# Optimization experiments

Measured on AMD Instinct MI355X. Metric: run time of the kernel, lower is better.

Reference implementation:

```python
import jax, jax.numpy as jnp
import numpy as np

RANK = 32
W0 = 30.0


def lip_linear(x, w, c, b=None):
    # LipschitzLinear: scale rows of w so row-wise L1 norm <= softplus(c)
    scale = jnp.minimum(jax.nn.softplus(c) / jnp.sum(jnp.abs(w), axis=-1), 1.0)
    y = x @ (w * scale[:, None]).T
    return y + b if b is not None else y


def setup_inputs() -> dict:
    key = jax.random.key(0)
    ks = jax.random.split(key, 20)
    d = {}
    d['coords'] = jax.random.normal(ks[0], (8, 32768, 3), dtype=jnp.float32)
    d['latents'] = jax.random.normal(ks[1], (8, 128), dtype=jnp.float32)
    d['nf_w_first'] = jax.random.normal(ks[2], (256, 3), dtype=jnp.float32)
    d['nf_b_first'] = jax.random.normal(ks[3], (256,), dtype=jnp.float32)
    d['nf_c_first'] = jax.random.uniform(ks[4], (1,), dtype=jnp.float32)
    d['nf_w_hid'] = jax.random.normal(ks[5], (3, 256, 256), dtype=jnp.float32)
    d['nf_b_hid'] = jax.random.normal(ks[6], (3, 256), dtype=jnp.float32)
    d['nf_c_hid'] = jax.random.uniform(ks[7], (3,), dtype=jnp.float32)
    d['nf_w_last'] = jax.random.normal(ks[8], (1, 256), dtype=jnp.float32)
    d['nf_b_last'] = jax.random.normal(ks[9], (1,), dtype=jnp.float32)
    d['nf_c_last'] = jax.random.uniform(ks[10], (1,), dtype=jnp.float32)
    d['Aw_first'] = jax.random.normal(ks[11], (96, 128), dtype=jnp.float32)
    d['Ac_first'] = jax.random.uniform(ks[12], (1,), dtype=jnp.float32)
    d['Aw_hid'] = jax.random.normal(ks[13], (3, 8192, 128), dtype=jnp.float32)
    d['Ac_hid'] = jax.random.uniform(ks[14], (3,), dtype=jnp.float32)
    d['Bw'] = jax.random.normal(ks[15], (4, 8192, 128), dtype=jnp.float32)
    d['Bc'] = jax.random.uniform(ks[16], (4,), dtype=jnp.float32)
    d['hbw'] = jax.random.normal(ks[17], (4, 256, 128), dtype=jnp.float32)
    d['hbc'] = jax.random.uniform(ks[18], (4,), dtype=jnp.float32)
    return d


def reference(coords, latents, nf_w_first, nf_b_first, nf_c_first, nf_w_hid, nf_b_hid, nf_c_hid,
              nf_w_last, nf_b_last, nf_c_last, Aw_first, Ac_first, Aw_hid, Ac_hid, Bw, Bc, hbw, hbc):
    T = latents.shape[0]
    # assemble per-layer params: (nf_w, nf_b, nf_c, A_w, A_c, B_w, B_c, hb_w, hb_c)
    layers = [(nf_w_first, nf_b_first, nf_c_first, Aw_first, Ac_first, Bw[0], Bc[0], hbw[0], hbc[0])]
    for j in range(nf_w_hid.shape[0]):
        layers.append((nf_w_hid[j], nf_b_hid[j], nf_c_hid[j], Aw_hid[j], Ac_hid[j],
                       Bw[j + 1], Bc[j + 1], hbw[j + 1], hbc[j + 1]))

    x = coords  # [T, N, d_in]
    for (w, b, c, aw, ac, bw, bc, hw, hc) in layers:
        d_out, d_in = w.shape
        A = lip_linear(latents, aw, ac).reshape(T, d_in, RANK)   # [T, d_in, r]
        B = lip_linear(latents, bw, bc).reshape(T, RANK, d_out)  # [T, r, d_out]
        bias = lip_linear(latents, hw, hc)                       # [T, d_out]
        base = lip_linear(x, w, c, b)                            # [T, N, d_out]
        mod = jnp.einsum('tnr,tro->tno', jnp.einsum('tni,tir->tnr', x, A), B)
        x = jnp.sin(W0 * (base + mod + bias[:, None, :]))
    return lip_linear(x, nf_w_last, nf_c_last, nf_b_last)  # [T, N, 1]
```

## Files before the change

### kernel.cpp

```cpp
#include <hip/hip_runtime.h>
#include <math.h>

#define W0F 30.0f
#define NPTS 32768

#define C_30_OVER_2PI 4.774648292756860070
#define C_2PI         6.283185307179586477

typedef double v4d __attribute__((ext_vector_type(4)));

#define OFF_M     0ull
#define SZ_M      2097152ull
#define OFF_CB    (OFF_M + SZ_M)
#define SZ_CB     8192ull
#define OFF_AF    (OFF_CB + SZ_CB)
#define SZ_AF     262144ull
#define OFF_BF    (OFF_AF + SZ_AF)
#define SZ_BF     262144ull
#define OFF_HB    (OFF_BF + SZ_BF)
#define SZ_HB     8192ull
#define OFF_NSC   (OFF_HB + SZ_HB)
#define SZ_NSC    2048ull
#define OFF_BSWZ  (OFF_NSC + SZ_NSC)
#define SZ_BSWZ   2097152ull
#define OFF_X0    (OFF_BSWZ + SZ_BSWZ)

__global__ __launch_bounds__(256) void setup1(
    const float* __restrict__ latents,
    const float* __restrict__ AwF, const float* __restrict__ AcF,
    const float* __restrict__ AwH, const float* __restrict__ AcH,
    const float* __restrict__ Bw,  const float* __restrict__ Bc,
    const float* __restrict__ hbw, const float* __restrict__ hbc,
    const float* __restrict__ wF,  const float* __restrict__ cF,
    const float* __restrict__ wH,  const float* __restrict__ cH,
    const float* __restrict__ wL,  const float* __restrict__ cL,
    float* __restrict__ AF, float* __restrict__ BFo,
    float* __restrict__ HBo, float* __restrict__ NSC)
{
    __shared__ float lat[1024];
    int tid = threadIdx.x;
    for (int j = tid; j < 1024; j += 256) lat[j] = latents[j];
    __syncthreads();
    int g = blockIdx.x * 256 + tid;
    if (g < 58464) {
        const float* src; float c; float* dst; int stride;
        if (g < 96) {
            src = AwF + g * 128; c = AcF[0]; dst = AF + g; stride = 8192;
        } else if (g < 24672) {
            int q = g - 96; int l = 1 + q / 8192;
            src = AwH + (size_t)q * 128; c = AcH[l - 1];
            dst = AF + (size_t)l * 8 * 8192 + (q % 8192); stride = 8192;
        } else if (g < 57440) {
            int q = g - 24672; int l = q / 8192;
            src = Bw + (size_t)q * 128; c = Bc[l];
            dst = BFo + (size_t)l * 8 * 8192 + (q % 8192); stride = 8192;
        } else {
            int q = g - 57440; int l = q / 256;
            src = hbw + (size_t)q * 128; c = hbc[l];
            dst = HBo + l * 8 * 256 + (q % 256); stride = 256;
        }
        double l1 = 0.0;
        double acc[8] = {0,0,0,0,0,0,0,0};
        for (int kk = 0; kk < 32; ++kk) {
            float4 w4 = ((const float4*)src)[kk];
            l1 += fabs((double)w4.x) + fabs((double)w4.y)
                + fabs((double)w4.z) + fabs((double)w4.w);
            int k = kk * 4;
            #pragma unroll
            for (int t = 0; t < 8; ++t) {
                const float* lp = &lat[t * 128 + k];
                acc[t] = fma((double)w4.x, (double)lp[0], acc[t]);
                acc[t] = fma((double)w4.y, (double)lp[1], acc[t]);
                acc[t] = fma((double)w4.z, (double)lp[2], acc[t]);
                acc[t] = fma((double)w4.w, (double)lp[3], acc[t]);
            }
        }
        double s = fmin(log1p(exp((double)c)) / l1, 1.0);
        #pragma unroll
        for (int t = 0; t < 8; ++t) dst[(size_t)t * stride] = (float)(acc[t] * s);
    } else if (g < 59489) {
        int h = g - 58464;
        if (h < 256) {
            const float* src = wF + h * 3;
            double l1 = fabs((double)src[0]) + fabs((double)src[1]) + fabs((double)src[2]);
            NSC[h] = (float)fmin(log1p(exp((double)cF[0])) / l1, 1.0);
        } else if (h < 1024) {
            int q = h - 256; int l = 1 + q / 256;
            const float* src = wH + (size_t)q * 256;
            double l1 = 0.0;
            for (int kk = 0; kk < 64; ++kk) {
                float4 w4 = ((const float4*)src)[kk];
                l1 += fabs((double)w4.x) + fabs((double)w4.y)
                    + fabs((double)w4.z) + fabs((double)w4.w);
            }
            NSC[256 + q] = (float)fmin(log1p(exp((double)cH[l - 1])) / l1, 1.0);
        } else {
            double l1 = 0.0;
            for (int kk = 0; kk < 64; ++kk) {
                float4 w4 = ((const float4*)wL)[kk];
                l1 += fabs((double)w4.x) + fabs((double)w4.y)
                    + fabs((double)w4.z) + fabs((double)w4.w);
            }
            NSC[1024] = (float)fmin(log1p(exp((double)cL[0])) / l1, 1.0);
        }
    }
}

__global__ __launch_bounds__(256) void setup2(
    const float* __restrict__ wF, const float* __restrict__ bF,
    const float* __restrict__ wH, const float* __restrict__ bH,
    const float* __restrict__ AF, const float* __restrict__ BFi,
    const float* __restrict__ HBi, const float* __restrict__ NSC,
    float* __restrict__ Mb, float* __restrict__ CBb)
{
    int b = blockIdx.x; int t = b / 49; int rem = b % 49;
    int o = threadIdx.x;
    int l, i0, ni;
    if (rem == 0) { l = 0; i0 = 0; ni = 3; }
    else { l = 1 + (rem - 1) / 16; i0 = ((rem - 1) % 16) * 16; ni = 16; }
    size_t ltb = (size_t)(l * 8 + t);
    const float* af = AF + ltb * 8192;
    const float* bf = BFi + ltb * 8192;
    double sc = (double)NSC[l * 256 + o];
    float bcol[32];
    #pragma unroll
    for (int r = 0; r < 32; ++r) bcol[r] = bf[r * 256 + o];
    for (int ii = 0; ii < ni; ++ii) {
        int i = i0 + ii;
        float wv = (l == 0) ? wF[o * 3 + i] : wH[(size_t)((l - 1) * 256 + o) * 256 + i];
        double m = (double)wv * sc;
        #pragma unroll
        for (int r = 0; r < 32; ++r)
            m = fma((double)af[i * 32 + r], (double)bcol[r], m);
        Mb[ltb * 65536 + (size_t)i * 256 + o] = (float)m;
    }
    if (rem == 0 || ((rem - 1) % 16) == 0) {
        double bb = (l == 0) ? (double)bF[o] : (double)bH[(l - 1) * 256 + o];
        CBb[ltb * 256 + o] = (float)(bb + (double)HBi[ltb * 256 + o]);
    }
}

__global__ __launch_bounds__(256) void setup3(
    const float* __restrict__ Mb, float* __restrict__ Bswz)
{
    int gid = blockIdx.x * 256 + threadIdx.x;
    int e    = gid & 3;
    int lane = (gid >> 2) & 63;
    int h    = (gid >> 8) & 1;
    int s    = (gid >> 9) & 63;
    int ltc  = gid >> 15;
    int q = lane >> 4, c16 = lane & 15;
    int ltb = ltc >> 1, ch = ltc & 1;
    int n = h * 4 + e;
    Bswz[gid] = Mb[(size_t)ltb * 65536 + (size_t)(4 * s + q) * 256
                   + ch * 128 + n * 16 + c16];
}

__device__ __forceinline__ float sin30(double z) {
    double u = z * C_30_OVER_2PI;
    double r = u - rint(u);
    return sinf((float)(r * C_2PI));
}

__global__ __launch_bounds__(256) void layer0_k(
    const float* __restrict__ coords, const float* __restrict__ Mb,
    const float* __restrict__ CBb, float* __restrict__ X, int tbase)
{
    __shared__ float Ms[3][256];
    __shared__ float cbs[256];
    int tid = threadIdx.x;
    int tl = blockIdx.x >> 10; int rb = blockIdx.x & 1023;
    int t = tbase + tl;
    const float* Mt = Mb + (size_t)t * 65536;
    Ms[0][tid] = Mt[tid]; Ms[1][tid] = Mt[256 + tid]; Ms[2][tid] = Mt[512 + tid];
    cbs[tid] = CBb[t * 256 + tid];
    __syncthreads();
    int r = rb * 32 + (tid >> 3); int lane8 = tid & 7;
    const float* cp = coords + ((size_t)t * NPTS + r) * 3;
    double c0 = (double)cp[0], c1 = (double)cp[1], c2 = (double)cp[2];
    float* xo = X + ((size_t)tl * NPTS + r) * 256;
#define L0E(col) sin30(fma(c2, (double)Ms[2][col], fma(c1, (double)Ms[1][col], \
                  fma(c0, (double)Ms[0][col], (double)cbs[col]))))
    #pragma unroll
    for (int j = 0; j < 8; ++j) {
        int col = 4 * lane8 + 32 * j;
        float4 v;
        v.x = L0E(col + 0);
        v.y = L0E(col + 1);
        v.z = L0E(col + 2);
        v.w = L0E(col + 3);
        *(float4*)(xo + col) = v;
    }
#undef L0E
}

__global__ __launch_bounds__(256, 4) void gemm_sin(
    const float* __restrict__ Xsrc, float* __restrict__ Xdst,
    const float* __restrict__ Bswz, const float* __restrict__ CBb,
    int l, int tbase)
{
    int tid = threadIdx.x;
    int b = blockIdx.x;
    int tl = b >> 10;
    int rb = (b >> 1) & 511;
    int ch = b & 1;
    size_t ltb = (size_t)(l * 8 + tbase + tl);
    const float* cbp = CBb + ltb * 256 + ch * 128;
    const float* Xs = Xsrc + ((size_t)tl * NPTS + rb * 64) * 256;
    float*       Xd = Xdst + ((size_t)tl * NPTS + rb * 64) * 256 + ch * 128;
    int wave = tid >> 6, lane = tid & 63;
    int q = lane >> 4, c16 = lane & 15;
    v4d zz = {0., 0., 0., 0.};
    v4d p1 = __builtin_amdgcn_mfma_f64_16x16x4f64((double)(1 << c16), 1.0, zz, 0, 0, 0);
    v4d p2 = __builtin_amdgcn_mfma_f64_16x16x4f64(1.0, (double)(1 << c16), zz, 0, 0, 0);
    int r0 = 61 - __builtin_clzll((unsigned long long)p1[0]);
    int r1 = 61 - __builtin_clzll((unsigned long long)p1[1]);
    int r2 = 61 - __builtin_clzll((unsigned long long)p1[2]);
    int r3 = 61 - __builtin_clzll((unsigned long long)p1[3]);
    int c0 = 61 - __builtin_clzll((unsigned long long)p2[0]);
    int c1 = 61 - __builtin_clzll((unsigned long long)p2[1]);
    int c2 = 61 - __builtin_clzll((unsigned long long)p2[2]);
    int c3 = 61 - __builtin_clzll((unsigned long long)p2[3]);
    const float* ap  = Xs + (size_t)(wave * 16 + c16) * 256 + q;
    const float* bzl = Bswz + ((size_t)ltb * 2 + ch) * 32768 + lane * 4;
    v4d acc0 = {0.,0.,0.,0.}, acc1 = {0.,0.,0.,0.}, acc2 = {0.,0.,0.,0.},
        acc3 = {0.,0.,0.,0.}, acc4 = {0.,0.,0.,0.}, acc5 = {0.,0.,0.,0.},
        acc6 = {0.,0.,0.,0.}, acc7 = {0.,0.,0.,0.};
    float  aC  = ap[0];
    float4 bC0 = *(const float4*)(bzl + 0 * 256);
    float4 bC1 = *(const float4*)(bzl + 1 * 256);
    float  aN  = ap[4];
    float4 bN0 = *(const float4*)(bzl + 2 * 256);
    float4 bN1 = *(const float4*)(bzl + 3 * 256);
    #pragma unroll 2
    for (int s = 0; s < 64; ++s) {
        int s2 = (s < 62) ? s + 2 : 63;
        float  aNN  = ap[4 * s2];
        float4 bNN0 = *(const float4*)(bzl + (s2 * 2 + 0) * 256);
        float4 bNN1 = *(const float4*)(bzl + (s2 * 2 + 1) * 256);
        double av = (double)aC;
#define TILE(n, bf) { acc##n = __builtin_amdgcn_mfma_f64_16x16x4f64(          \
                               av, (double)(bf), acc##n, 0, 0, 0); }
        TILE(0, bC0.x) TILE(1, bC0.y) TILE(2, bC0.z) TILE(3, bC0.w)
        TILE(4, bC1.x) TILE(5, bC1.y) TILE(6, bC1.z) TILE(7, bC1.w)
#undef TILE
        aC = aN;  aN = aNN;
        bC0 = bN0; bC1 = bN1; bN0 = bNN0; bN1 = bNN1;
    }
    float* Xw = Xd + (size_t)(wave * 16) * 256;
#define EPT(n) {                                                               \
        int cb0 = (n) * 16;                                                    \
        Xw[r0 * 256 + cb0 + c0] = sin30(acc##n[0] + (double)cbp[cb0 + c0]);    \
        Xw[r1 * 256 + cb0 + c1] = sin30(acc##n[1] + (double)cbp[cb0 + c1]);    \
        Xw[r2 * 256 + cb0 + c2] = sin30(acc##n[2] + (double)cbp[cb0 + c2]);    \
        Xw[r3 * 256 + cb0 + c3] = sin30(acc##n[3] + (double)cbp[cb0 + c3]); }
    EPT(0) EPT(1) EPT(2) EPT(3)
    EPT(4) EPT(5) EPT(6) EPT(7)
#undef EPT
}

__global__ __launch_bounds__(256) void final_k(
    const float* __restrict__ X, const float* __restrict__ wl,
    const float* __restrict__ bl, const float* __restrict__ NSC,
    float* __restrict__ out, int tbase)
{
    int tid = threadIdx.x; int w = tid >> 6; int lane = tid & 63;
    size_t row = (size_t)blockIdx.x * 4 + w;
    double ls = (double)NSC[1024];
    float4 wv = ((const float4*)wl)[lane];
    float4 xv = *(const float4*)(X + row * 256 + lane * 4);
    double d = 0.0;
    d = fma((double)wv.x, (double)xv.x, d);
    d = fma((double)wv.y, (double)xv.y, d);
    d = fma((double)wv.z, (double)xv.z, d);
    d = fma((double)wv.w, (double)xv.w, d);
    d *= ls;
    #pragma unroll
    for (int off = 32; off > 0; off >>= 1) d += __shfl_down(d, off, 64);
    if (lane == 0) out[(size_t)tbase * NPTS + row] = (float)(d + (double)bl[0]);
}

extern "C" void kernel_launch(void* const* d_in, const int* in_sizes, int n_in,
                              void* d_out, int out_size, void* d_ws, size_t ws_size,
                              hipStream_t stream)
{
    const float* coords     = (const float*)d_in[0];
    const float* latents    = (const float*)d_in[1];
    const float* nf_w_first = (const float*)d_in[2];
    const float* nf_b_first = (const float*)d_in[3];
    const float* nf_c_first = (const float*)d_in[4];
    const float* nf_w_hid   = (const float*)d_in[5];
    const float* nf_b_hid   = (const float*)d_in[6];
    const float* nf_c_hid   = (const float*)d_in[7];
    const float* nf_w_last  = (const float*)d_in[8];
    const float* nf_b_last  = (const float*)d_in[9];
    const float* nf_c_last  = (const float*)d_in[10];
    const float* Aw_first   = (const float*)d_in[11];
    const float* Ac_first   = (const float*)d_in[12];
    const float* Aw_hid     = (const float*)d_in[13];
    const float* Ac_hid     = (const float*)d_in[14];
    const float* Bw         = (const float*)d_in[15];
    const float* Bc         = (const float*)d_in[16];
    const float* hbw        = (const float*)d_in[17];
    const float* hbc        = (const float*)d_in[18];

    float* ws  = (float*)d_ws;
    float* Mb  = ws + OFF_M;
    float* CBb = ws + OFF_CB;
    float* AF  = ws + OFF_AF;
    float* BFb = ws + OFF_BF;
    float* HBb = ws + OFF_HB;
    float* NSC = ws + OFF_NSC;
    float* Bz  = ws + OFF_BSWZ;
    float* out = (float*)d_out;

    size_t availf = ws_size / sizeof(float);
    size_t xslice = (size_t)NPTS * 256;
    int T = 2;
    if (availf >= OFF_X0 + 2ull * 8 * xslice)      T = 8;
    else if (availf >= OFF_X0 + 2ull * 4 * xslice) T = 4;
    float* X0 = ws + OFF_X0;
    float* X1 = X0 + (size_t)T * xslice;

    setup1<<<233, 256, 0, stream>>>(latents, Aw_first, Ac_first, Aw_hid, Ac_hid,
                                    Bw, Bc, hbw, hbc,
                                    nf_w_first, nf_c_first, nf_w_hid, nf_c_hid,
                                    nf_w_last, nf_c_last,
                                    AF, BFb, HBb, NSC);
    setup2<<<392, 256, 0, stream>>>(nf_w_first, nf_b_first, nf_w_hid, nf_b_hid,
                                    AF, BFb, HBb, NSC, Mb, CBb);
    setup3<<<8192, 256, 0, stream>>>(Mb, Bz);
    for (int tbase = 0; tbase < 8; tbase += T) {
        layer0_k<<<1024 * T, 256, 0, stream>>>(coords, Mb, CBb, X0, tbase);
        gemm_sin<<<1024 * T, 256, 0, stream>>>(X0, X1, Bz, CBb, 1, tbase);
        gemm_sin<<<1024 * T, 256, 0, stream>>>(X1, X0, Bz, CBb, 2, tbase);
        gemm_sin<<<1024 * T, 256, 0, stream>>>(X0, X1, Bz, CBb, 3, tbase);
        final_k<<<T * 8192, 256, 0, stream>>>(X1, nf_w_last, nf_b_last, NSC, out, tbase);
    }
}
```

Before: 2.095 ms.

## Store intermediate activations in MFMA-fragment order for coalesced A-operand loads

Activations between layers are now written in a swizzled layout where each 16-row by 4-column A fragment is contiguous. The GEMM kernel can then load its A operand with a per-lane stride-1 access instead of strided row reads. The prefetch depth in the k-loop grows from two to three stages. The epilogue writes the swizzled layout for intermediate layers and keeps the row-major layout for the last GEMM, which feeds final_k. The cost is scattered scalar stores in layer0 and the epilogue, plus more live registers from the deeper prefetch.

After: 2.260 ms. 7.9% more time.

```diff
diff --git a/kernel.cpp b/kernel.cpp
--- a/kernel.cpp
+++ b/kernel.cpp
@@ -178,18 +178,18 @@
     int r = rb * 32 + (tid >> 3); int lane8 = tid & 7;
     const float* cp = coords + ((size_t)t * NPTS + r) * 3;
     double c0 = (double)cp[0], c1 = (double)cp[1], c2 = (double)cp[2];
-    float* xo = X + ((size_t)tl * NPTS + r) * 256;
+    float* xo = X + (size_t)tl * NPTS * 256 + (size_t)(r >> 4) * 4096 + (r & 15);
 #define L0E(col) sin30(fma(c2, (double)Ms[2][col], fma(c1, (double)Ms[1][col], \
                   fma(c0, (double)Ms[0][col], (double)cbs[col]))))
     #pragma unroll
     for (int j = 0; j < 8; ++j) {
         int col = 4 * lane8 + 32 * j;
-        float4 v;
-        v.x = L0E(col + 0);
-        v.y = L0E(col + 1);
-        v.z = L0E(col + 2);
-        v.w = L0E(col + 3);
-        *(float4*)(xo + col) = v;
+        int cs  = lane8 + 8 * j;
+        float* p = xo + cs * 64;
+        p[0]  = L0E(col + 0);
+        p[16] = L0E(col + 1);
+        p[32] = L0E(col + 2);
+        p[48] = L0E(col + 3);
     }
 #undef L0E
 }
@@ -197,7 +197,7 @@
 __global__ __launch_bounds__(256, 4) void gemm_sin(
     const float* __restrict__ Xsrc, float* __restrict__ Xdst,
     const float* __restrict__ Bswz, const float* __restrict__ CBb,
-    int l, int tbase)
+    int l, int tbase, int swz_out)
 {
     int tid = threadIdx.x;
     int b = blockIdx.x;
@@ -206,10 +206,37 @@
     int ch = b & 1;
     size_t ltb = (size_t)(l * 8 + tbase + tl);
     const float* cbp = CBb + ltb * 256 + ch * 128;
-    const float* Xs = Xsrc + ((size_t)tl * NPTS + rb * 64) * 256;
-    float*       Xd = Xdst + ((size_t)tl * NPTS + rb * 64) * 256 + ch * 128;
     int wave = tid >> 6, lane = tid & 63;
     int q = lane >> 4, c16 = lane & 15;
+    const float* ap = Xsrc + (size_t)tl * NPTS * 256 + (size_t)rb * 16384
+                    + (size_t)wave * 4096 + lane;
+    const float* bzl = Bswz + ((size_t)ltb * 2 + ch) * 32768 + lane * 4;
+    v4d acc0 = {0.,0.,0.,0.}, acc1 = {0.,0.,0.,0.}, acc2 = {0.,0.,0.,0.},
+        acc3 = {0.,0.,0.,0.}, acc4 = {0.,0.,0.,0.}, acc5 = {0.,0.,0.,0.},
+        acc6 = {0.,0.,0.,0.}, acc7 = {0.,0.,0.,0.};
+    float  a0 = ap[0];
+    float4 b00 = *(const float4*)(bzl + 0 * 256);
+    float4 b10 = *(const float4*)(bzl + 1 * 256);
+    float  a1 = ap[64];
+    float4 b01 = *(const float4*)(bzl + 2 * 256);
+    float4 b11 = *(const float4*)(bzl + 3 * 256);
+    float  a2 = ap[128];
+    float4 b02 = *(const float4*)(bzl + 4 * 256);
+    float4 b12 = *(const float4*)(bzl + 5 * 256);
+    #pragma unroll 3
+    for (int s = 0; s < 64; ++s) {
+        double av = (double)a0;
+#define TILE(n, bf) { acc##n = __builtin_amdgcn_mfma_f64_16x16x4f64(          \
+                               av, (double)(bf), acc##n, 0, 0, 0); }
+        TILE(0, b00.x) TILE(1, b00.y) TILE(2, b00.z) TILE(3, b00.w)
+        TILE(4, b10.x) TILE(5, b10.y) TILE(6, b10.z) TILE(7, b10.w)
+#undef TILE
+        int sp = (s < 61) ? s + 3 : 63;
+        a0 = a1; a1 = a2; a2 = ap[64 * sp];
+        b00 = b01; b10 = b11; b01 = b02; b11 = b12;
+        b02 = *(const float4*)(bzl + (size_t)(2 * sp + 0) * 256);
+        b12 = *(const float4*)(bzl + (size_t)(2 * sp + 1) * 256);
+    }
     v4d zz = {0., 0., 0., 0.};
     v4d p1 = __builtin_amdgcn_mfma_f64_16x16x4f64((double)(1 << c16), 1.0, zz, 0, 0, 0);
     v4d p2 = __builtin_amdgcn_mfma_f64_16x16x4f64(1.0, (double)(1 << c16), zz, 0, 0, 0);
@@ -221,42 +248,37 @@
     int c1 = 61 - __builtin_clzll((unsigned long long)p2[1]);
     int c2 = 61 - __builtin_clzll((unsigned long long)p2[2]);
     int c3 = 61 - __builtin_clzll((unsigned long long)p2[3]);
-    const float* ap  = Xs + (size_t)(wave * 16 + c16) * 256 + q;
-    const float* bzl = Bswz + ((size_t)ltb * 2 + ch) * 32768 + lane * 4;
-    v4d acc0 = {0.,0.,0.,0.}, acc1 = {0.,0.,0.,0.}, acc2 = {0.,0.,0.,0.},
-        acc3 = {0.,0.,0.,0.}, acc4 = {0.,0.,0.,0.}, acc5 = {0.,0.,0.,0.},
-        acc6 = {0.,0.,0.,0.}, acc7 = {0.,0.,0.,0.};
-    float  aC  = ap[0];
-    float4 bC0 = *(const float4*)(bzl + 0 * 256);
-    float4 bC1 = *(const float4*)(bzl + 1 * 256);
-    float  aN  = ap[4];
-    float4 bN0 = *(const float4*)(bzl + 2 * 256);
-    float4 bN1 = *(const float4*)(bzl + 3 * 256);
-    #pragma unroll 2
-    for (int s = 0; s < 64; ++s) {
-        int s2 = (s < 62) ? s + 2 : 63;
-        float  aNN  = ap[4 * s2];
-        float4 bNN0 = *(const float4*)(bzl + (s2 * 2 + 0) * 256);
-        float4 bNN1 = *(const float4*)(bzl + (s2 * 2 + 1) * 256);
-        double av = (double)aC;
-#define TILE(n, bf) { acc##n = __builtin_amdgcn_mfma_f64_16x16x4f64(          \
-                               av, (double)(bf), acc##n, 0, 0, 0); }
-        TILE(0, bC0.x) TILE(1, bC0.y) TILE(2, bC0.z) TILE(3, bC0.w)
-        TILE(4, bC1.x) TILE(5, bC1.y) TILE(6, bC1.z) TILE(7, bC1.w)
-#undef TILE
-        aC = aN;  aN = aNN;
-        bC0 = bN0; bC1 = bN1; bN0 = bNN0; bN1 = bNN1;
-    }
-    float* Xw = Xd + (size_t)(wave * 16) * 256;
+
+    if (swz_out) {
+        float* Xw = Xdst + (size_t)tl * NPTS * 256 + (size_t)rb * 16384
+                  + (size_t)wave * 4096 + (size_t)ch * 2048;
+        int o0 = (c0 >> 2) * 64 + (c0 & 3) * 16 + r0;
+        int o1 = (c1 >> 2) * 64 + (c1 & 3) * 16 + r1;
+        int o2 = (c2 >> 2) * 64 + (c2 & 3) * 16 + r2;
+        int o3 = (c3 >> 2) * 64 + (c3 & 3) * 16 + r3;
+#define EPTS(n) {                                                              \
+        int cb0 = (n) * 16;                                                    \
+        float* Pn = Xw + (n) * 256;                                            \
+        Pn[o0] = sin30(acc##n[0] + (double)cbp[cb0 + c0]);                     \
+        Pn[o1] = sin30(acc##n[1] + (double)cbp[cb0 + c1]);                     \
+        Pn[o2] = sin30(acc##n[2] + (double)cbp[cb0 + c2]);                     \
+        Pn[o3] = sin30(acc##n[3] + (double)cbp[cb0 + c3]); }
+        EPTS(0) EPTS(1) EPTS(2) EPTS(3)
+        EPTS(4) EPTS(5) EPTS(6) EPTS(7)
+#undef EPTS
+    } else {
+        float* Xw = Xdst + ((size_t)tl * NPTS + (size_t)rb * 64) * 256
+                  + ch * 128 + (size_t)(wave * 16) * 256;
 #define EPT(n) {                                                               \
         int cb0 = (n) * 16;                                                    \
         Xw[r0 * 256 + cb0 + c0] = sin30(acc##n[0] + (double)cbp[cb0 + c0]);    \
         Xw[r1 * 256 + cb0 + c1] = sin30(acc##n[1] + (double)cbp[cb0 + c1]);    \
         Xw[r2 * 256 + cb0 + c2] = sin30(acc##n[2] + (double)cbp[cb0 + c2]);    \
         Xw[r3 * 256 + cb0 + c3] = sin30(acc##n[3] + (double)cbp[cb0 + c3]); }
-    EPT(0) EPT(1) EPT(2) EPT(3)
-    EPT(4) EPT(5) EPT(6) EPT(7)
+        EPT(0) EPT(1) EPT(2) EPT(3)
+        EPT(4) EPT(5) EPT(6) EPT(7)
 #undef EPT
+    }
 }
 
 __global__ __launch_bounds__(256) void final_k(
@@ -332,9 +354,9 @@
     setup3<<<8192, 256, 0, stream>>>(Mb, Bz);
     for (int tbase = 0; tbase < 8; tbase += T) {
         layer0_k<<<1024 * T, 256, 0, stream>>>(coords, Mb, CBb, X0, tbase);
-        gemm_sin<<<1024 * T, 256, 0, stream>>>(X0, X1, Bz, CBb, 1, tbase);
-        gemm_sin<<<1024 * T, 256, 0, stream>>>(X1, X0, Bz, CBb, 2, tbase);
-        gemm_sin<<<1024 * T, 256, 0, stream>>>(X0, X1, Bz, CBb, 3, tbase);
+        gemm_sin<<<1024 * T, 256, 0, stream>>>(X0, X1, Bz, CBb, 1, tbase, 1);
+        gemm_sin<<<1024 * T, 256, 0, stream>>>(X1, X0, Bz, CBb, 2, tbase, 1);
+        gemm_sin<<<1024 * T, 256, 0, stream>>>(X0, X1, Bz, CBb, 3, tbase, 0);
         final_k<<<T * 8192, 256, 0, stream>>>(X1, nf_w_last, nf_b_last, NSC, out, tbase);
     }
 }
```
